# Kernel optimization log

Hardware: AMD Instinct MI355X
Metric: run time of the kernel (lower is better)

The kernel has to match this reference:

```python
import jax, jax.numpy as jnp
import numpy as np

DIM = 768
HEADS = 12
DIM_HEAD = 64
INNER = HEADS * DIM_HEAD  # 768
SCALE = DIM_HEAD ** -0.5


def setup_inputs() -> dict:
    key = jax.random.key(0)
    k1, k2, k3, k4 = jax.random.split(key, 4)
    x = jax.random.normal(k1, (4, 1024, DIM), dtype=jnp.float32)
    # nn.Linear weights stored as [out, in]; we keep [in, out] for x @ W.
    w_qkv = jax.random.normal(k2, (DIM, 3 * INNER), dtype=jnp.float32) * (DIM ** -0.5)
    w_out = jax.random.normal(k3, (INNER, DIM), dtype=jnp.float32) * (INNER ** -0.5)
    b_out = jax.random.normal(k4, (DIM,), dtype=jnp.float32) * 0.02
    return {"x": x, "w_qkv": w_qkv, "w_out": w_out, "b_out": b_out}


def reference(x, w_qkv, w_out, b_out):
    B, N, _ = x.shape
    qkv = x @ w_qkv  # [B, N, 3*inner]
    q, k, v = jnp.split(qkv, 3, axis=-1)
    # b n (h d) -> b h n d
    def to_heads(t):
        return t.reshape(B, N, HEADS, DIM_HEAD).transpose(0, 2, 1, 3)
    q, k, v = to_heads(q), to_heads(k), to_heads(v)
    dots = jnp.einsum('bhnd,bhmd->bhnm', q, k) * SCALE  # [B, H, N, N]
    attn = jax.nn.softmax(dots, axis=-1)  # dropout p=0 -> identity
    out = jnp.einsum('bhnm,bhmd->bhnd', attn, v)
    out = out.transpose(0, 2, 1, 3).reshape(B, N, INNER)  # b h n d -> b n (h d)
    return out @ w_out + b_out
```

## Files before the change

### kernel.cpp

```cpp
#include <hip/hip_runtime.h>
#include <math.h>


typedef __attribute__((ext_vector_type(8))) __bf16 bf16x8;
typedef __attribute__((ext_vector_type(4))) float f32x4;
typedef __attribute__((ext_vector_type(16))) float f32x16;
typedef unsigned short u16;
typedef unsigned int u32;

#define ZERO16 {0,0,0,0,0,0,0,0,0,0,0,0,0,0,0,0}

__device__ __forceinline__ u16 f2bf(float f) {
    union { float f; unsigned u; } v; v.f = f;
    unsigned r = v.u + 0x7FFF + ((v.u >> 16) & 1);
    return (u16)(r >> 16);
}

__device__ __forceinline__ u32 cvtpk(float lo, float hi) {
    u32 r;
    asm("v_cvt_pk_bf16_f32 %0, %1, %2" : "=v"(r) : "v"(lo), "v"(hi));
    return r;
}
__device__ __forceinline__ float xhalf_max(float x) {
    float o = __shfl_xor(x, 32);
    return fmaxf(x, o);
}
__device__ __forceinline__ float xhalf_sum(float x) {
    float o = __shfl_xor(x, 32);
    return x + o;
}

__device__ __forceinline__ size_t fragoff(int m, int k) {
    return (((size_t)(m >> 4) * 24 + (k >> 5)) * 64 + (m & 15) + 16 * ((k & 31) >> 3)) * 8 + (k & 7);
}

__global__ __launch_bounds__(256) void prep(const float* __restrict__ x,
                                            const float* __restrict__ w_qkv,
                                            const float* __restrict__ w_out,
                                            u16* __restrict__ xA,
                                            u16* __restrict__ wB,
                                            u16* __restrict__ wO) {
    const int bid = blockIdx.x;
    const int tid = threadIdx.x;
    if (bid < 1536) {
        __shared__ float Tx[32][65];
        const int mt = bid & 127;
        const int kt = bid >> 7;
        const int r0 = mt * 32, k0 = kt * 64;
#pragma unroll
        for (int p = 0; p < 2; ++p) {
            int idx = tid + p * 256;
            int row = idx >> 4, c4 = idx & 15;
            float4 v = *reinterpret_cast<const float4*>(&x[(size_t)(r0 + row) * 768 + k0 + c4 * 4]);
            *reinterpret_cast<float4*>(&Tx[row][c4 * 4]) = v;
        }
        __syncthreads();
        const int f = tid >> 6, l = tid & 63;
        const int fm = f & 1, fk = f >> 1;
        const int lm = l & 15, lkc = l >> 4;
        const int lrow = fm * 16 + lm;
        const int lcol = fk * 32 + lkc * 8;
        float v0 = Tx[lrow][lcol + 0], v1 = Tx[lrow][lcol + 1];
        float v2 = Tx[lrow][lcol + 2], v3 = Tx[lrow][lcol + 3];
        float v4 = Tx[lrow][lcol + 4], v5 = Tx[lrow][lcol + 5];
        float v6 = Tx[lrow][lcol + 6], v7 = Tx[lrow][lcol + 7];
        int4 ov;
        ov.x = (int)cvtpk(v0, v1); ov.y = (int)cvtpk(v2, v3);
        ov.z = (int)cvtpk(v4, v5); ov.w = (int)cvtpk(v6, v7);
        *reinterpret_cast<int4*>(xA + fragoff(r0 + lrow, k0 + lcol)) = ov;
        return;
    }
    __shared__ float T[32][33];
    const float* in;
    u16* out;
    int C, c0, r0;
    if (bid < 3264) {
        int r = bid - 1536;
        in = w_qkv; out = wB; C = 2304;
        c0 = (r % 72) * 32; r0 = (r / 72) * 32;
    } else {
        int r = bid - 3264;
        in = w_out; out = wO; C = 768;
        c0 = (r % 24) * 32; r0 = (r / 24) * 32;
    }
    const int tx = tid & 31;
    const int ty = tid >> 5;
#pragma unroll
    for (int p = 0; p < 4; ++p) {
        int ry = ty + p * 8;
        T[ry][tx] = in[(size_t)(r0 + ry) * C + c0 + tx];
    }
    __syncthreads();
#pragma unroll
    for (int p = 0; p < 4; ++p) {
        int cy = ty + p * 8;
        out[fragoff(c0 + cy, r0 + tx)] = f2bf(T[tx][cy]);
    }
}

__global__ __launch_bounds__(256) void gemm_qkv(const u16* __restrict__ xA,
                                                const u16* __restrict__ wB,
                                                u16* __restrict__ Qf,
                                                u16* __restrict__ Kf,
                                                u16* __restrict__ Vf) {
    const int tid = threadIdx.x;
    const int lane = tid & 63;
    const int w = tid >> 6;
    const int wm = w >> 1, wn = w & 1;
    const int lr = lane & 15;
    const int lk = lane >> 4;
    const int xcd = blockIdx.x & 7;
    const int lid = blockIdx.x >> 3;
    const int row0 = ((xcd & 3) * 8 + (lid & 7)) * 128;
    const int col0 = ((xcd >> 2) * 9 + (lid >> 3)) * 128;
    const int R0 = row0 + wm * 64;
    const int C0 = col0 + wn * 64;
    const u16* aB = xA + (size_t)(R0 >> 4) * 24 * 512 + lane * 8;
    const u16* bB = wB + (size_t)(C0 >> 4) * 24 * 512 + lane * 8;

    f32x4 acc[4][4];
#pragma unroll
    for (int mi = 0; mi < 4; ++mi)
#pragma unroll
        for (int nj = 0; nj < 4; ++nj) acc[mi][nj] = (f32x4){0.f, 0.f, 0.f, 0.f};

    int4 ra[3][4], rb[3][4];
#define LOADF(S, T)                                                           \
    {                                                                         \
        _Pragma("unroll")                                                     \
        for (int mi = 0; mi < 4; ++mi) {                                      \
            ra[S][mi] = *reinterpret_cast<const int4*>(aB + ((size_t)mi * 24 + (T)) * 512); \
            rb[S][mi] = *reinterpret_cast<const int4*>(bB + ((size_t)mi * 24 + (T)) * 512); \
        }                                                                     \
    }
#define COMPUTEF(S)                                                           \
    {                                                                         \
        union { int4 i; bf16x8 v; } af[4], bf[4];                             \
        _Pragma("unroll")                                                     \
        for (int mi = 0; mi < 4; ++mi) { af[mi].i = ra[S][mi]; bf[mi].i = rb[S][mi]; } \
        __builtin_amdgcn_s_setprio(1);                                        \
        _Pragma("unroll")                                                     \
        for (int mi = 0; mi < 4; ++mi)                                        \
            _Pragma("unroll")                                                 \
            for (int nj = 0; nj < 4; ++nj)                                    \
                acc[mi][nj] = __builtin_amdgcn_mfma_f32_16x16x32_bf16(af[mi].v, bf[nj].v, acc[mi][nj], 0, 0, 0); \
        __builtin_amdgcn_s_setprio(0);                                        \
    }

    LOADF(0, 0);
    LOADF(1, 1);
    LOADF(2, 2);
#pragma unroll
    for (int t = 0; t < 24; ++t) {
        COMPUTEF(t % 3);
        if (t + 3 < 24) { LOADF(t % 3, t + 3); }
    }
#undef LOADF
#undef COMPUTEF

    const int which = col0 / 768;
    const int cb = col0 - which * 768;
#pragma unroll
    for (int mi = 0; mi < 4; ++mi) {
#pragma unroll
        for (int i = 0; i < 4; ++i) {
            int r = row0 + wm * 64 + mi * 16 + lk * 4 + i;
            int b = r >> 10, n = r & 1023;
#pragma unroll
            for (int nj = 0; nj < 4; ++nj) {
                int cw = cb + wn * 64 + nj * 16 + lr;
                int h = cw >> 6, d = cw & 63;
                int bh = b * 12 + h;
                float val = acc[mi][nj][i];
                if (which == 2) {
                    size_t off = ((((size_t)bh * 16 + (n >> 6)) * 4 + ((n >> 4) & 3)) * 2 + ((n >> 3) & 1)) * 512
                                 + d * 8 + (n & 7);
                    Vf[off] = f2bf(val);
                } else {
                    size_t off = ((((size_t)bh * 32 + (n >> 5)) * 4 + (d >> 4)) * 2 + ((d >> 3) & 1)) * 256
                                 + (n & 31) * 8 + (d & 7);
                    if (which == 0) Qf[off] = f2bf(val * 0.18033688f);
                    else            Kf[off] = f2bf(val);
                }
            }
        }
    }
}

#define GETO(dt, r) ((dt) == 0 ? o0[r] : o1[r])

__global__ __launch_bounds__(256) void attn_mfma(const u16* __restrict__ Qf,
                                                 const u16* __restrict__ Kf,
                                                 const u16* __restrict__ Vf,
                                                 u16* __restrict__ attnF) {
    __shared__ float OtM[2][64][33];
    __shared__ float Lm[2][32], Ll[2][32];
    __shared__ u16 Os[2][32][72];

    const int tid = threadIdx.x;
    const int lane = tid & 63;
    const int w = tid >> 6;
    const int qsub = w & 1;
    const int half = w >> 1;
    const int l31 = lane & 31;
    const int hi = lane >> 5;

    const int bid = blockIdx.x;
    const int lin = (bid & 7) * 96 + (bid >> 3);
    const int qt = lin & 15;
    const int bh = lin >> 4;

    const u16* Qh = Qf + (size_t)bh * 65536;
    const u16* Kh = Kf + (size_t)bh * 65536;
    const u16* Vh = Vf + (size_t)bh * 65536;

    bf16x8 qf[4];
#pragma unroll
    for (int kt = 0; kt < 4; ++kt)
        qf[kt] = *reinterpret_cast<const bf16x8*>(
            Qh + (((size_t)(qt * 2 + qsub) * 4 + kt) * 2 + hi) * 256 + l31 * 8);

    f32x16 o0 = ZERO16, o1 = ZERO16;
    float m = -1e30f, l = 0.f;

    for (int it = 0; it < 8; ++it) {
        const int kb0 = it * 4 + half * 2;
        const int kvb = it * 2 + half;

        bf16x8 kf0[4], kf1[4];
#pragma unroll
        for (int kt = 0; kt < 4; ++kt) {
            kf0[kt] = *reinterpret_cast<const bf16x8*>(
                Kh + (((size_t)kb0 * 4 + kt) * 2 + hi) * 256 + l31 * 8);
            kf1[kt] = *reinterpret_cast<const bf16x8*>(
                Kh + (((size_t)(kb0 + 1) * 4 + kt) * 2 + hi) * 256 + l31 * 8);
        }
        bf16x8 vf0[4], vf1[4];
#pragma unroll
        for (int ks = 0; ks < 4; ++ks) {
            const u16* vb = Vh + (((size_t)kvb * 4 + ks) * 2 + hi) * 512;
            vf0[ks] = *reinterpret_cast<const bf16x8*>(vb + l31 * 8);
            vf1[ks] = *reinterpret_cast<const bf16x8*>(vb + (l31 + 32) * 8);
        }

        f32x16 s0 = ZERO16, s1 = ZERO16;
        __builtin_amdgcn_s_setprio(1);
#pragma unroll
        for (int kt = 0; kt < 4; ++kt) s0 = __builtin_amdgcn_mfma_f32_32x32x16_bf16(kf0[kt], qf[kt], s0, 0, 0, 0);
#pragma unroll
        for (int kt = 0; kt < 4; ++kt) s1 = __builtin_amdgcn_mfma_f32_32x32x16_bf16(kf1[kt], qf[kt], s1, 0, 0, 0);
        __builtin_amdgcn_s_setprio(0);

        float mx[8];
#pragma unroll
        for (int i = 0; i < 8; ++i)
            mx[i] = fmaxf(fmaxf(s0[2*i], s0[2*i+1]), fmaxf(s1[2*i], s1[2*i+1]));
        float pmax = fmaxf(fmaxf(fmaxf(mx[0], mx[1]), fmaxf(mx[2], mx[3])),
                           fmaxf(fmaxf(mx[4], mx[5]), fmaxf(mx[6], mx[7])));
        pmax = xhalf_max(pmax);

        if (!__all(pmax <= m + 8.f)) {
            float mn = fmaxf(m, pmax);
            float c = __builtin_amdgcn_exp2f(m - mn);
            m = mn; l *= c;
            o0 = o0 * c; o1 = o1 * c;
        }

#pragma unroll
        for (int r = 0; r < 16; ++r) s0[r] = __builtin_amdgcn_exp2f(s0[r] - m);
#pragma unroll
        for (int r = 0; r < 16; ++r) s1[r] = __builtin_amdgcn_exp2f(s1[r] - m);
        float sm[8];
#pragma unroll
        for (int i = 0; i < 8; ++i)
            sm[i] = (s0[2*i] + s0[2*i+1]) + (s1[2*i] + s1[2*i+1]);
        float tsum = ((sm[0]+sm[1]) + (sm[2]+sm[3])) + ((sm[4]+sm[5]) + (sm[6]+sm[7]));
        l += xhalf_sum(tsum);

        bf16x8 pb[4];
#define PACK_GROUP(S, G, OUT)                                           \
        {                                                               \
            u32 X0 = cvtpk(S[8*(G)+0], S[8*(G)+1]);                     \
            u32 X1 = cvtpk(S[8*(G)+2], S[8*(G)+3]);                     \
            u32 Y0 = cvtpk(S[8*(G)+4], S[8*(G)+5]);                     \
            u32 Y1 = cvtpk(S[8*(G)+6], S[8*(G)+7]);                     \
            u32 X0s = (u32)__shfl_xor((int)X0, 32);                     \
            u32 X1s = (u32)__shfl_xor((int)X1, 32);                     \
            u32 Y0s = (u32)__shfl_xor((int)Y0, 32);                     \
            u32 Y1s = (u32)__shfl_xor((int)Y1, 32);                     \
            union { u32 u[4]; bf16x8 v; } pk_;                          \
            pk_.u[0] = hi ? Y0s : X0;                                   \
            pk_.u[1] = hi ? Y1s : X1;                                   \
            pk_.u[2] = hi ? Y0 : X0s;                                   \
            pk_.u[3] = hi ? Y1 : X1s;                                   \
            OUT = pk_.v;                                                \
        }
        PACK_GROUP(s0, 0, pb[0]);
        PACK_GROUP(s0, 1, pb[1]);
        PACK_GROUP(s1, 0, pb[2]);
        PACK_GROUP(s1, 1, pb[3]);
#undef PACK_GROUP

        __builtin_amdgcn_s_setprio(1);
#pragma unroll
        for (int ks = 0; ks < 4; ++ks) {
            o0 = __builtin_amdgcn_mfma_f32_32x32x16_bf16(vf0[ks], pb[ks], o0, 0, 0, 0);
            o1 = __builtin_amdgcn_mfma_f32_32x32x16_bf16(vf1[ks], pb[ks], o1, 0, 0, 0);
        }
        __builtin_amdgcn_s_setprio(0);
    }

    if (half == 1) {
#pragma unroll
        for (int dt = 0; dt < 2; ++dt)
#pragma unroll
            for (int r = 0; r < 16; ++r)
                OtM[qsub][dt * 32 + (r & 3) + 8 * (r >> 2) + 4 * hi][l31] = GETO(dt, r);
        Lm[qsub][l31] = m;
        Ll[qsub][l31] = l;
    }
    __syncthreads();
    if (half == 0) {
        float m2 = Lm[qsub][l31], l2 = Ll[qsub][l31];
        float mn = fmaxf(m, m2);
        float a = __builtin_amdgcn_exp2f(m - mn);
        float bsc = __builtin_amdgcn_exp2f(m2 - mn);
        float lm = l * a + l2 * bsc;
        float inv = 1.0f / lm;
        float av = a * inv, bv = bsc * inv;
#pragma unroll
        for (int dt = 0; dt < 2; ++dt)
#pragma unroll
            for (int rq = 0; rq < 4; ++rq) {
                int d0 = dt * 32 + 8 * rq + 4 * hi;
                float v0 = GETO(dt, rq * 4 + 0) * av + OtM[qsub][d0 + 0][l31] * bv;
                float v1 = GETO(dt, rq * 4 + 1) * av + OtM[qsub][d0 + 1][l31] * bv;
                float v2 = GETO(dt, rq * 4 + 2) * av + OtM[qsub][d0 + 2][l31] * bv;
                float v3 = GETO(dt, rq * 4 + 3) * av + OtM[qsub][d0 + 3][l31] * bv;
                uint2 pr;
                pr.x = cvtpk(v0, v1);
                pr.y = cvtpk(v2, v3);
                *reinterpret_cast<uint2*>(&Os[qsub][l31][d0]) = pr;
            }
    }
    __syncthreads();

    const int b = bh / 12, h = bh % 12;
#pragma unroll
    for (int it2 = 0; it2 < 2; ++it2) {
        int idx = tid + it2 * 256;
        int token = idx >> 3;
        int chunk = idx & 7;
        int4 v = *reinterpret_cast<const int4*>(&Os[token >> 5][token & 31][chunk * 8]);
        int mm = b * 1024 + qt * 64 + token;
        int kk = h * 64 + chunk * 8;
        *reinterpret_cast<int4*>(attnF + fragoff(mm, kk)) = v;
    }
}

__global__ __launch_bounds__(256) void gemm_out(const u16* __restrict__ attnF,
                                                const u16* __restrict__ wO,
                                                const float* __restrict__ bias,
                                                float* __restrict__ out) {
    const int tid = threadIdx.x;
    const int lane = tid & 63;
    const int w = tid >> 6;
    const int wm = w >> 1, wn = w & 1;
    const int lr = lane & 15;
    const int lk = lane >> 4;
    const int xcd = blockIdx.x & 7;
    const int lid = blockIdx.x >> 3;
    const int row0 = (xcd * 4 + (lid & 3)) * 128;
    const int col0 = (lid >> 2) * 128;
    const int R0 = row0 + wm * 64;
    const int C0 = col0 + wn * 64;
    const u16* aB = attnF + (size_t)(R0 >> 4) * 24 * 512 + lane * 8;
    const u16* bB = wO + (size_t)(C0 >> 4) * 24 * 512 + lane * 8;

    f32x4 acc[4][4];
#pragma unroll
    for (int mi = 0; mi < 4; ++mi)
#pragma unroll
        for (int nj = 0; nj < 4; ++nj) acc[mi][nj] = (f32x4){0.f, 0.f, 0.f, 0.f};

    int4 ra[3][4], rb[3][4];
#define LOADF(S, T)                                                           \
    {                                                                         \
        _Pragma("unroll")                                                     \
        for (int mi = 0; mi < 4; ++mi) {                                      \
            ra[S][mi] = *reinterpret_cast<const int4*>(aB + ((size_t)mi * 24 + (T)) * 512); \
            rb[S][mi] = *reinterpret_cast<const int4*>(bB + ((size_t)mi * 24 + (T)) * 512); \
        }                                                                     \
    }
#define COMPUTEF(S)                                                           \
    {                                                                         \
        union { int4 i; bf16x8 v; } af[4], bf[4];                             \
        _Pragma("unroll")                                                     \
        for (int mi = 0; mi < 4; ++mi) { af[mi].i = ra[S][mi]; bf[mi].i = rb[S][mi]; } \
        __builtin_amdgcn_s_setprio(1);                                        \
        _Pragma("unroll")                                                     \
        for (int mi = 0; mi < 4; ++mi)                                        \
            _Pragma("unroll")                                                 \
            for (int nj = 0; nj < 4; ++nj)                                    \
                acc[mi][nj] = __builtin_amdgcn_mfma_f32_16x16x32_bf16(af[mi].v, bf[nj].v, acc[mi][nj], 0, 0, 0); \
        __builtin_amdgcn_s_setprio(0);                                        \
    }

    LOADF(0, 0);
    LOADF(1, 1);
    LOADF(2, 2);
#pragma unroll
    for (int t = 0; t < 24; ++t) {
        COMPUTEF(t % 3);
        if (t + 3 < 24) { LOADF(t % 3, t + 3); }
    }
#undef LOADF
#undef COMPUTEF

#pragma unroll
    for (int mi = 0; mi < 4; ++mi)
#pragma unroll
        for (int i = 0; i < 4; ++i) {
            int r = row0 + wm * 64 + mi * 16 + lk * 4 + i;
#pragma unroll
            for (int nj = 0; nj < 4; ++nj) {
                int c = col0 + wn * 64 + nj * 16 + lr;
                out[(size_t)r * 768 + c] = acc[mi][nj][i] + bias[c];
            }
        }
}

extern "C" void kernel_launch(void* const* d_in, const int* in_sizes, int n_in,
                              void* d_out, int out_size, void* d_ws, size_t ws_size,
                              hipStream_t stream) {
    const float* x     = (const float*)d_in[0];
    const float* w_qkv = (const float*)d_in[1];
    const float* w_out = (const float*)d_in[2];
    const float* b_out = (const float*)d_in[3];
    float* out = (float*)d_out;

    u16* ws = (u16*)d_ws;
    const size_t n_x = (size_t)4096 * 768;
    u16* xA     = ws;
    u16* wB     = xA + n_x;
    u16* wO     = wB + (size_t)2304 * 768;
    u16* Qfr    = wO + (size_t)768 * 768;
    u16* Kfr    = Qfr + n_x;
    u16* Vfr    = Kfr + n_x;
    u16* attnF  = Vfr + n_x;

    prep<<<3840, 256, 0, stream>>>(x, w_qkv, w_out, xA, wB, wO);
    gemm_qkv<<<576, 256, 0, stream>>>(xA, wB, Qfr, Kfr, Vfr);
    attn_mfma<<<768, 256, 0, stream>>>(Qfr, Kfr, Vfr, attnF);
    gemm_out<<<192, 256, 0, stream>>>(attnF, wO, b_out, out);
}
```

Baseline: 78.95 us.

## Retile weight prep, split GEMMs into single-wave blocks, prefetch K in attention

The weight-conversion part of prep now uses 64x64 tiles and writes packed 8-element bf16 vectors, which cuts the block count and replaces scalar stores with wide stores. Both projection GEMMs are relaunched as one-wave 64x64-tile blocks, four times as many blocks, to spread the work over more CUs; each block now reads its A and B tiles without reuse across waves. The attention loop double-buffers the K fragments so the next tile's K loads are issued right after the QK MFMAs and overlap the softmax. Double-buffering adds register pressure.

```diff
diff --git a/kernel.cpp b/kernel.cpp
--- a/kernel.cpp
+++ b/kernel.cpp
@@ -70,53 +70,55 @@
         *reinterpret_cast<int4*>(xA + fragoff(r0 + lrow, k0 + lcol)) = ov;
         return;
     }
-    __shared__ float T[32][33];
+    __shared__ float T[64][65];
     const float* in;
     u16* out;
-    int C, c0, r0;
-    if (bid < 3264) {
+    int C, n0, k0;
+    if (bid < 1968) {
         int r = bid - 1536;
         in = w_qkv; out = wB; C = 2304;
-        c0 = (r % 72) * 32; r0 = (r / 72) * 32;
+        n0 = (r % 36) * 64; k0 = (r / 36) * 64;
     } else {
-        int r = bid - 3264;
+        int r = bid - 1968;
         in = w_out; out = wO; C = 768;
-        c0 = (r % 24) * 32; r0 = (r / 24) * 32;
-    }
-    const int tx = tid & 31;
-    const int ty = tid >> 5;
-#pragma unroll
-    for (int p = 0; p < 4; ++p) {
-        int ry = ty + p * 8;
-        T[ry][tx] = in[(size_t)(r0 + ry) * C + c0 + tx];
+        n0 = (r % 12) * 64; k0 = (r / 12) * 64;
+    }
+#pragma unroll
+    for (int p = 0; p < 16; ++p) {
+        int idx = tid + p * 256;
+        int row = idx >> 6, col = idx & 63;
+        T[row][col] = in[(size_t)(k0 + row) * C + n0 + col];
     }
     __syncthreads();
 #pragma unroll
-    for (int p = 0; p < 4; ++p) {
-        int cy = ty + p * 8;
-        out[fragoff(c0 + cy, r0 + tx)] = f2bf(T[tx][cy]);
-    }
-}
-
-__global__ __launch_bounds__(256) void gemm_qkv(const u16* __restrict__ xA,
-                                                const u16* __restrict__ wB,
-                                                u16* __restrict__ Qf,
-                                                u16* __restrict__ Kf,
-                                                u16* __restrict__ Vf) {
-    const int tid = threadIdx.x;
-    const int lane = tid & 63;
-    const int w = tid >> 6;
-    const int wm = w >> 1, wn = w & 1;
+    for (int q = 0; q < 2; ++q) {
+        int lin = tid + q * 256;
+        int nl = lin >> 3, kc = lin & 7;
+        float v0 = T[kc * 8 + 0][nl], v1 = T[kc * 8 + 1][nl];
+        float v2 = T[kc * 8 + 2][nl], v3 = T[kc * 8 + 3][nl];
+        float v4 = T[kc * 8 + 4][nl], v5 = T[kc * 8 + 5][nl];
+        float v6 = T[kc * 8 + 6][nl], v7 = T[kc * 8 + 7][nl];
+        int4 ov;
+        ov.x = (int)cvtpk(v0, v1); ov.y = (int)cvtpk(v2, v3);
+        ov.z = (int)cvtpk(v4, v5); ov.w = (int)cvtpk(v6, v7);
+        *reinterpret_cast<int4*>(out + fragoff(n0 + nl, k0 + kc * 8)) = ov;
+    }
+}
+
+__global__ __launch_bounds__(64) void gemm_qkv(const u16* __restrict__ xA,
+                                               const u16* __restrict__ wB,
+                                               u16* __restrict__ Qf,
+                                               u16* __restrict__ Kf,
+                                               u16* __restrict__ Vf) {
+    const int lane = threadIdx.x;
     const int lr = lane & 15;
     const int lk = lane >> 4;
     const int xcd = blockIdx.x & 7;
     const int lid = blockIdx.x >> 3;
-    const int row0 = ((xcd & 3) * 8 + (lid & 7)) * 128;
-    const int col0 = ((xcd >> 2) * 9 + (lid >> 3)) * 128;
-    const int R0 = row0 + wm * 64;
-    const int C0 = col0 + wn * 64;
-    const u16* aB = xA + (size_t)(R0 >> 4) * 24 * 512 + lane * 8;
-    const u16* bB = wB + (size_t)(C0 >> 4) * 24 * 512 + lane * 8;
+    const int row0 = ((xcd & 3) * 16 + (lid & 15)) * 64;
+    const int col0 = ((xcd >> 2) * 18 + (lid >> 4)) * 64;
+    const u16* aB = xA + (size_t)(row0 >> 4) * 24 * 512 + lane * 8;
+    const u16* bB = wB + (size_t)(col0 >> 4) * 24 * 512 + lane * 8;
 
     f32x4 acc[4][4];
 #pragma unroll
@@ -164,11 +166,11 @@
     for (int mi = 0; mi < 4; ++mi) {
 #pragma unroll
         for (int i = 0; i < 4; ++i) {
-            int r = row0 + wm * 64 + mi * 16 + lk * 4 + i;
+            int r = row0 + mi * 16 + lk * 4 + i;
             int b = r >> 10, n = r & 1023;
 #pragma unroll
             for (int nj = 0; nj < 4; ++nj) {
-                int cw = cb + wn * 64 + nj * 16 + lr;
+                int cw = cb + nj * 16 + lr;
                 int h = cw >> 6, d = cw & 63;
                 int bh = b * 12 + h;
                 float val = acc[mi][nj][i];
@@ -223,61 +225,75 @@
     f32x16 o0 = ZERO16, o1 = ZERO16;
     float m = -1e30f, l = 0.f;
 
-    for (int it = 0; it < 8; ++it) {
-        const int kb0 = it * 4 + half * 2;
-        const int kvb = it * 2 + half;
-
-        bf16x8 kf0[4], kf1[4];
-#pragma unroll
-        for (int kt = 0; kt < 4; ++kt) {
-            kf0[kt] = *reinterpret_cast<const bf16x8*>(
-                Kh + (((size_t)kb0 * 4 + kt) * 2 + hi) * 256 + l31 * 8);
-            kf1[kt] = *reinterpret_cast<const bf16x8*>(
-                Kh + (((size_t)(kb0 + 1) * 4 + kt) * 2 + hi) * 256 + l31 * 8);
-        }
-        bf16x8 vf0[4], vf1[4];
-#pragma unroll
-        for (int ks = 0; ks < 4; ++ks) {
-            const u16* vb = Vh + (((size_t)kvb * 4 + ks) * 2 + hi) * 512;
-            vf0[ks] = *reinterpret_cast<const bf16x8*>(vb + l31 * 8);
-            vf1[ks] = *reinterpret_cast<const bf16x8*>(vb + (l31 + 32) * 8);
-        }
-
-        f32x16 s0 = ZERO16, s1 = ZERO16;
-        __builtin_amdgcn_s_setprio(1);
-#pragma unroll
-        for (int kt = 0; kt < 4; ++kt) s0 = __builtin_amdgcn_mfma_f32_32x32x16_bf16(kf0[kt], qf[kt], s0, 0, 0, 0);
-#pragma unroll
-        for (int kt = 0; kt < 4; ++kt) s1 = __builtin_amdgcn_mfma_f32_32x32x16_bf16(kf1[kt], qf[kt], s1, 0, 0, 0);
-        __builtin_amdgcn_s_setprio(0);
-
-        float mx[8];
-#pragma unroll
-        for (int i = 0; i < 8; ++i)
-            mx[i] = fmaxf(fmaxf(s0[2*i], s0[2*i+1]), fmaxf(s1[2*i], s1[2*i+1]));
-        float pmax = fmaxf(fmaxf(fmaxf(mx[0], mx[1]), fmaxf(mx[2], mx[3])),
-                           fmaxf(fmaxf(mx[4], mx[5]), fmaxf(mx[6], mx[7])));
-        pmax = xhalf_max(pmax);
-
-        if (!__all(pmax <= m + 8.f)) {
-            float mn = fmaxf(m, pmax);
-            float c = __builtin_amdgcn_exp2f(m - mn);
-            m = mn; l *= c;
-            o0 = o0 * c; o1 = o1 * c;
-        }
-
-#pragma unroll
-        for (int r = 0; r < 16; ++r) s0[r] = __builtin_amdgcn_exp2f(s0[r] - m);
-#pragma unroll
-        for (int r = 0; r < 16; ++r) s1[r] = __builtin_amdgcn_exp2f(s1[r] - m);
-        float sm[8];
-#pragma unroll
-        for (int i = 0; i < 8; ++i)
-            sm[i] = (s0[2*i] + s0[2*i+1]) + (s1[2*i] + s1[2*i+1]);
-        float tsum = ((sm[0]+sm[1]) + (sm[2]+sm[3])) + ((sm[4]+sm[5]) + (sm[6]+sm[7]));
-        l += xhalf_sum(tsum);
-
-        bf16x8 pb[4];
+    bf16x8 k0a[4], k0b[4], k1a[4], k1b[4];
+
+#define LOADK(KA, KB, IT)                                                     \
+    {                                                                         \
+        const int kb0_ = (IT) * 4 + half * 2;                                 \
+        _Pragma("unroll")                                                     \
+        for (int kt = 0; kt < 4; ++kt) {                                      \
+            KA[kt] = *reinterpret_cast<const bf16x8*>(                        \
+                Kh + (((size_t)kb0_ * 4 + kt) * 2 + hi) * 256 + l31 * 8);     \
+            KB[kt] = *reinterpret_cast<const bf16x8*>(                        \
+                Kh + (((size_t)(kb0_ + 1) * 4 + kt) * 2 + hi) * 256 + l31 * 8); \
+        }                                                                     \
+    }
+
+#define ATTN_BODY(IT, KCA, KCB, KNA, KNB)                                     \
+    {                                                                         \
+        const int kvb = (IT) * 2 + half;                                      \
+        bf16x8 vf0[4], vf1[4];                                                \
+        _Pragma("unroll")                                                     \
+        for (int ks = 0; ks < 4; ++ks) {                                      \
+            const u16* vb = Vh + (((size_t)kvb * 4 + ks) * 2 + hi) * 512;     \
+            vf0[ks] = *reinterpret_cast<const bf16x8*>(vb + l31 * 8);         \
+            vf1[ks] = *reinterpret_cast<const bf16x8*>(vb + (l31 + 32) * 8);  \
+        }                                                                     \
+        f32x16 s0 = ZERO16, s1 = ZERO16;                                      \
+        __builtin_amdgcn_s_setprio(1);                                        \
+        _Pragma("unroll")                                                     \
+        for (int kt = 0; kt < 4; ++kt) s0 = __builtin_amdgcn_mfma_f32_32x32x16_bf16(KCA[kt], qf[kt], s0, 0, 0, 0); \
+        _Pragma("unroll")                                                     \
+        for (int kt = 0; kt < 4; ++kt) s1 = __builtin_amdgcn_mfma_f32_32x32x16_bf16(KCB[kt], qf[kt], s1, 0, 0, 0); \
+        __builtin_amdgcn_s_setprio(0);                                        \
+        if ((IT) < 7) { LOADK(KNA, KNB, (IT) + 1); }                          \
+        float mx[8];                                                          \
+        _Pragma("unroll")                                                     \
+        for (int i = 0; i < 8; ++i)                                           \
+            mx[i] = fmaxf(fmaxf(s0[2*i], s0[2*i+1]), fmaxf(s1[2*i], s1[2*i+1])); \
+        float pmax = fmaxf(fmaxf(fmaxf(mx[0], mx[1]), fmaxf(mx[2], mx[3])),   \
+                           fmaxf(fmaxf(mx[4], mx[5]), fmaxf(mx[6], mx[7])));  \
+        pmax = xhalf_max(pmax);                                               \
+        if (!__all(pmax <= m + 8.f)) {                                        \
+            float mn = fmaxf(m, pmax);                                        \
+            float c = __builtin_amdgcn_exp2f(m - mn);                         \
+            m = mn; l *= c;                                                   \
+            o0 = o0 * c; o1 = o1 * c;                                         \
+        }                                                                     \
+        _Pragma("unroll")                                                     \
+        for (int r = 0; r < 16; ++r) s0[r] = __builtin_amdgcn_exp2f(s0[r] - m); \
+        _Pragma("unroll")                                                     \
+        for (int r = 0; r < 16; ++r) s1[r] = __builtin_amdgcn_exp2f(s1[r] - m); \
+        float sm[8];                                                          \
+        _Pragma("unroll")                                                     \
+        for (int i = 0; i < 8; ++i)                                           \
+            sm[i] = (s0[2*i] + s0[2*i+1]) + (s1[2*i] + s1[2*i+1]);            \
+        float tsum = ((sm[0]+sm[1]) + (sm[2]+sm[3])) + ((sm[4]+sm[5]) + (sm[6]+sm[7])); \
+        l += xhalf_sum(tsum);                                                 \
+        bf16x8 pb[4];                                                         \
+        PACK_GROUP(s0, 0, pb[0]);                                             \
+        PACK_GROUP(s0, 1, pb[1]);                                             \
+        PACK_GROUP(s1, 0, pb[2]);                                             \
+        PACK_GROUP(s1, 1, pb[3]);                                             \
+        __builtin_amdgcn_s_setprio(1);                                        \
+        _Pragma("unroll")                                                     \
+        for (int ks = 0; ks < 4; ++ks) {                                      \
+            o0 = __builtin_amdgcn_mfma_f32_32x32x16_bf16(vf0[ks], pb[ks], o0, 0, 0, 0); \
+            o1 = __builtin_amdgcn_mfma_f32_32x32x16_bf16(vf1[ks], pb[ks], o1, 0, 0, 0); \
+        }                                                                     \
+        __builtin_amdgcn_s_setprio(0);                                        \
+    }
+
 #define PACK_GROUP(S, G, OUT)                                           \
         {                                                               \
             u32 X0 = cvtpk(S[8*(G)+0], S[8*(G)+1]);                     \
@@ -295,20 +311,16 @@
             pk_.u[3] = hi ? Y1 : X1s;                                   \
             OUT = pk_.v;                                                \
         }
-        PACK_GROUP(s0, 0, pb[0]);
-        PACK_GROUP(s0, 1, pb[1]);
-        PACK_GROUP(s1, 0, pb[2]);
-        PACK_GROUP(s1, 1, pb[3]);
+
+    LOADK(k0a, k0b, 0);
+#pragma unroll 1
+    for (int ii = 0; ii < 8; ii += 2) {
+        ATTN_BODY(ii, k0a, k0b, k1a, k1b);
+        ATTN_BODY(ii + 1, k1a, k1b, k0a, k0b);
+    }
+#undef ATTN_BODY
 #undef PACK_GROUP
-
-        __builtin_amdgcn_s_setprio(1);
-#pragma unroll
-        for (int ks = 0; ks < 4; ++ks) {
-            o0 = __builtin_amdgcn_mfma_f32_32x32x16_bf16(vf0[ks], pb[ks], o0, 0, 0, 0);
-            o1 = __builtin_amdgcn_mfma_f32_32x32x16_bf16(vf1[ks], pb[ks], o1, 0, 0, 0);
-        }
-        __builtin_amdgcn_s_setprio(0);
-    }
+#undef LOADK
 
     if (half == 1) {
 #pragma unroll
@@ -358,24 +370,19 @@
     }
 }
 
-__global__ __launch_bounds__(256) void gemm_out(const u16* __restrict__ attnF,
-                                                const u16* __restrict__ wO,
-                                                const float* __restrict__ bias,
-                                                float* __restrict__ out) {
-    const int tid = threadIdx.x;
-    const int lane = tid & 63;
-    const int w = tid >> 6;
-    const int wm = w >> 1, wn = w & 1;
+__global__ __launch_bounds__(64) void gemm_out(const u16* __restrict__ attnF,
+                                               const u16* __restrict__ wO,
+                                               const float* __restrict__ bias,
+                                               float* __restrict__ out) {
+    const int lane = threadIdx.x;
     const int lr = lane & 15;
     const int lk = lane >> 4;
     const int xcd = blockIdx.x & 7;
     const int lid = blockIdx.x >> 3;
-    const int row0 = (xcd * 4 + (lid & 3)) * 128;
-    const int col0 = (lid >> 2) * 128;
-    const int R0 = row0 + wm * 64;
-    const int C0 = col0 + wn * 64;
-    const u16* aB = attnF + (size_t)(R0 >> 4) * 24 * 512 + lane * 8;
-    const u16* bB = wO + (size_t)(C0 >> 4) * 24 * 512 + lane * 8;
+    const int row0 = (xcd * 8 + (lid & 7)) * 64;
+    const int col0 = (lid >> 3) * 64;
+    const u16* aB = attnF + (size_t)(row0 >> 4) * 24 * 512 + lane * 8;
+    const u16* bB = wO + (size_t)(col0 >> 4) * 24 * 512 + lane * 8;
 
     f32x4 acc[4][4];
 #pragma unroll
@@ -421,10 +428,10 @@
     for (int mi = 0; mi < 4; ++mi)
 #pragma unroll
         for (int i = 0; i < 4; ++i) {
-            int r = row0 + wm * 64 + mi * 16 + lk * 4 + i;
+            int r = row0 + mi * 16 + lk * 4 + i;
 #pragma unroll
             for (int nj = 0; nj < 4; ++nj) {
-                int c = col0 + wn * 64 + nj * 16 + lr;
+                int c = col0 + nj * 16 + lr;
                 out[(size_t)r * 768 + c] = acc[mi][nj][i] + bias[c];
             }
         }
@@ -449,8 +456,8 @@
     u16* Vfr    = Kfr + n_x;
     u16* attnF  = Vfr + n_x;
 
-    prep<<<3840, 256, 0, stream>>>(x, w_qkv, w_out, xA, wB, wO);
-    gemm_qkv<<<576, 256, 0, stream>>>(xA, wB, Qfr, Kfr, Vfr);
+    prep<<<2112, 256, 0, stream>>>(x, w_qkv, w_out, xA, wB, wO);
+    gemm_qkv<<<2304, 64, 0, stream>>>(xA, wB, Qfr, Kfr, Vfr);
     attn_mfma<<<768, 256, 0, stream>>>(Qfr, Kfr, Vfr, attnF);
-    gemm_out<<<192, 256, 0, stream>>>(attnF, wO, b_out, out);
-}
+    gemm_out<<<768, 64, 0, stream>>>(attnF, wO, b_out, out);
+}
```

New measurement: 80.89 us. 1.02x slower.
